# Optimization experiments

Measured on AMD Instinct MI355X. Metric: run time of the kernel, lower is better.

Reference implementation:

```python
import jax, jax.numpy as jnp
import numpy as np

H = 16  # num_heads

def setup_inputs() -> dict:
    key = jax.random.key(0)
    ks = jax.random.split(key, 9)
    B, S, E = 2, 2048, 1024
    d = E // H  # 64, shared KV head dim
    sc = lambda n: 1.0 / np.sqrt(n)
    return {
        "x": jax.random.normal(ks[0], (B, S, E), jnp.float32),
        "wq": jax.random.normal(ks[1], (E, E), jnp.float32) * sc(E),
        "bq": jax.random.normal(ks[2], (E,), jnp.float32) * 0.02,
        "wk": jax.random.normal(ks[3], (E, d), jnp.float32) * sc(E),
        "bk": jax.random.normal(ks[4], (d,), jnp.float32) * 0.02,
        "wv": jax.random.normal(ks[5], (E, d), jnp.float32) * sc(E),
        "bv": jax.random.normal(ks[6], (d,), jnp.float32) * 0.02,
        "wo": jax.random.normal(ks[7], (E, E), jnp.float32) * sc(E),
        "bo": jax.random.normal(ks[8], (E,), jnp.float32) * 0.02,
    }

def reference(x, wq, bq, wk, bk, wv, bv, wo, bo):
    B, S, E = x.shape
    d = E // H
    Q = (x @ wq + bq).reshape(B, S, H, d).transpose(0, 2, 1, 3)  # [B,H,S,d]
    K = x @ wk + bk  # [B,S,d] shared across heads (MQA)
    V = x @ wv + bv  # [B,S,d]
    scores = jnp.einsum('bhqd,bkd->bhqk', Q, K) / np.sqrt(d)  # [B,H,S,S]
    weights = jax.nn.softmax(scores, axis=-1)
    attn = jnp.einsum('bhqk,bkd->bhqd', weights, V)  # [B,H,S,d]
    # FAITHFUL to source: reshape [B,H,S,d] -> [B,S,E] WITHOUT permuting back
    attn = attn.reshape(B, S, E)
    return attn @ wo + bo
```

## Files before the change

### kernel.cpp

```cpp
#include <hip/hip_runtime.h>
#include <hip/hip_bf16.h>

#define BB 2
#define SS 2048
#define EE 1024
#define HH 16
#define DD 64

using bfrag = __attribute__((ext_vector_type(8))) short;
using ffrag = __attribute__((ext_vector_type(4))) float;

static __device__ __forceinline__ ushort f2bf(float f) {
  __hip_bfloat16 h = __float2bfloat16(f);
  return *reinterpret_cast<ushort*>(&h);
}

static __device__ __forceinline__ uint pack_bf2(float lo, float hi) {
  uint a = __float_as_uint(lo) + 0x8000u;
  uint b = __float_as_uint(hi) + 0x8000u;
  return __builtin_amdgcn_perm(b, a, 0x07060302u);
}

static __device__ __forceinline__ void gl_lds16(const ushort* g, ushort* l) {
  __builtin_amdgcn_global_load_lds(
      (const __attribute__((address_space(1))) void*)g,
      (__attribute__((address_space(3))) void*)l, 16, 0, 0);
}

__global__ __launch_bounds__(256) void cast_bf16_4(
    const float* __restrict__ src, ushort* __restrict__ dst, int n4) {
  int i = blockIdx.x * 256 + threadIdx.x;
  if (i < n4) {
    float4 v = ((const float4*)src)[i];
    ushort4 u = { f2bf(v.x), f2bf(v.y), f2bf(v.z), f2bf(v.w) };
    ((ushort4*)dst)[i] = u;
  }
}

__global__ __launch_bounds__(256) void transpose_cast(
    const float* __restrict__ src, ushort* __restrict__ dst, int K, int N) {
  __shared__ float t[32][33];
  const int k0 = blockIdx.y * 32, n0 = blockIdx.x * 32;
  const int tx = threadIdx.x & 31, ty = threadIdx.x >> 5;
  #pragma unroll
  for (int i = 0; i < 32; i += 8)
    t[ty + i][tx] = src[(size_t)(k0 + ty + i) * N + n0 + tx];
  __syncthreads();
  #pragma unroll
  for (int i = 0; i < 32; i += 8)
    dst[(size_t)(n0 + ty + i) * K + k0 + tx] = f2bf(t[tx][ty + i]);
}

template <bool QKV>
__global__ __launch_bounds__(256) void gemm_mfma3(
    const ushort* __restrict__ A, const ushort* __restrict__ Bt,
    const float* __restrict__ bias0, const float* __restrict__ bias1,
    const float* __restrict__ bias2, void* __restrict__ O1,
    ushort* __restrict__ O2, int M, int N, int K, float qscale) {
  __shared__ __align__(16) ushort As[2][128 * 64];
  __shared__ __align__(16) ushort Bs[2][64 * 64];
  const int tid = threadIdx.x;
  const int lane = tid & 63;
  const int quad = lane >> 4;
  const int c = lane & 15;
  const int wv = tid >> 6;
  const int wm = (wv & 1) * 64;
  const int wn = (wv >> 1) * 32;
  const size_t m0 = (size_t)blockIdx.y * 128;
  const size_t n0 = (size_t)blockIdx.x * 64;

  const int srow = lane >> 3;
  const int sck = (lane & 7) ^ srow;

  ffrag zero = {0.f, 0.f, 0.f, 0.f};
  ffrag acc[4][2];
  #pragma unroll
  for (int mt = 0; mt < 4; ++mt)
    #pragma unroll
    for (int nt = 0; nt < 2; ++nt) acc[mt][nt] = zero;

  const int NK = K >> 6;
  #pragma unroll
  for (int i = 0; i < 4; ++i) {
    int ia = wv * 4 + i;
    gl_lds16(&A[(m0 + ia * 8 + srow) * (size_t)K + sck * 8], &As[0][ia * 512]);
  }
  #pragma unroll
  for (int i = 0; i < 2; ++i) {
    int ib = wv * 2 + i;
    gl_lds16(&Bt[(n0 + ib * 8 + srow) * (size_t)K + sck * 8], &Bs[0][ib * 512]);
  }
  __syncthreads();

  for (int ki = 0; ki < NK; ++ki) {
    const int buf = ki & 1;
    if (ki + 1 < NK) {
      int k0 = (ki + 1) << 6;
      #pragma unroll
      for (int i = 0; i < 4; ++i) {
        int ia = wv * 4 + i;
        gl_lds16(&A[(m0 + ia * 8 + srow) * (size_t)K + k0 + sck * 8],
                 &As[buf ^ 1][ia * 512]);
      }
      #pragma unroll
      for (int i = 0; i < 2; ++i) {
        int ib = wv * 2 + i;
        gl_lds16(&Bt[(n0 + ib * 8 + srow) * (size_t)K + k0 + sck * 8],
                 &Bs[buf ^ 1][ib * 512]);
      }
    }
    #pragma unroll
    for (int ks = 0; ks < 2; ++ks) {
      bfrag af[4], bf[2];
      #pragma unroll
      for (int mt = 0; mt < 4; ++mt) {
        int ra = wm + mt * 16 + c;
        af[mt] = *(const bfrag*)&As[buf][(ra * 8 + ((ks * 4 + quad) ^ (ra & 7))) * 8];
      }
      #pragma unroll
      for (int nt = 0; nt < 2; ++nt) {
        int rb = wn + nt * 16 + c;
        bf[nt] = *(const bfrag*)&Bs[buf][(rb * 8 + ((ks * 4 + quad) ^ (rb & 7))) * 8];
      }
      #pragma unroll
      for (int mt = 0; mt < 4; ++mt)
        #pragma unroll
        for (int nt = 0; nt < 2; ++nt)
          acc[mt][nt] = __builtin_amdgcn_mfma_f32_16x16x32_bf16(
              af[mt], bf[nt], acc[mt][nt], 0, 0, 0);
    }
    __syncthreads();
  }

  #pragma unroll
  for (int nt = 0; nt < 2; ++nt) {
    const int colb = (int)n0 + wn + nt * 16;
    if (QKV) {
      float bb, sc;
      ushort* dst;
      int ldw;
      if (colb < 1024) {
        bb = bias0[colb + c]; sc = qscale;
        dst = (ushort*)O1 + colb; ldw = 1024;
      } else if (colb < 1088) {
        bb = bias1[colb - 1024 + c]; sc = 1.f;
        dst = O2 + (colb - 1024); ldw = 128;
      } else {
        bb = bias2[colb - 1088 + c]; sc = 1.f;
        dst = O2 + (colb - 1024); ldw = 128;
      }
      #pragma unroll
      for (int mt = 0; mt < 4; ++mt)
        #pragma unroll
        for (int r = 0; r < 4; ++r) {
          size_t row = m0 + wm + mt * 16 + quad * 4 + r;
          dst[row * ldw + c] = f2bf((acc[mt][nt][r] + bb) * sc);
        }
    } else {
      float bb = bias0[colb + c];
      float* dst = (float*)O1;
      #pragma unroll
      for (int mt = 0; mt < 4; ++mt)
        #pragma unroll
        for (int r = 0; r < 4; ++r) {
          size_t row = m0 + wm + mt * 16 + quad * 4 + r;
          dst[row * (size_t)N + colb + c] = acc[mt][nt][r] + bb;
        }
    }
  }
}

__global__ __launch_bounds__(256) void vt_pack(
    const ushort* __restrict__ KV, ushort* __restrict__ VT) {
  __shared__ ushort t[64][65];
  const int blk = blockIdx.x;
  const int b = blk >> 5;
  const int s0 = (blk & 31) << 6;
  const int tid = threadIdx.x;
  for (int e = tid; e < 4096; e += 256) {
    int si = e >> 6, di = e & 63;
    t[si][di] = KV[((size_t)(b * SS) + s0 + si) * 128 + 64 + di];
  }
  __syncthreads();
  for (int e = tid; e < 4096; e += 256) {
    int di = e >> 6, si = e & 63;
    VT[((size_t)b * 64 + di) * SS + s0 + si] = t[si][di];
  }
}

__global__ __launch_bounds__(256, 1) void mqa_attn7(
    const ushort* __restrict__ Q, const ushort* __restrict__ KV,
    const ushort* __restrict__ VT, ushort* __restrict__ A2) {
  __shared__ __align__(16) ushort Kt[2][4096];
  __shared__ __align__(16) ushort Vt[2][4096];
  __shared__ __align__(16) ushort P[4][64 * 72];
  const int tid = threadIdx.x;
  const int lane = tid & 63;
  const int quad = lane >> 4;
  const int c = lane & 15;
  const int wv = tid >> 6;
  const int bid = blockIdx.x;
  const int b = bid >> 7;
  const int r = bid & 127;
  const int h = r >> 3;
  const int s0 = (r & 7) << 8;

  const int srow = lane >> 3;
  const int sck = (lane & 7) ^ srow;

  ffrag zero = {0.f, 0.f, 0.f, 0.f};
  bfrag ones;
  #pragma unroll
  for (int i = 0; i < 8; ++i) ones[i] = (short)16256;

  bfrag aq[4][2];
  #pragma unroll
  for (int mt = 0; mt < 4; ++mt) {
    const ushort* qp =
        Q + ((size_t)(b * SS) + s0 + wv * 64 + mt * 16 + c) * EE + h * 64 + quad * 8;
    aq[mt][0] = *(const bfrag*)qp;
    aq[mt][1] = *(const bfrag*)(qp + 32);
  }

  ffrag o[4][4];
  #pragma unroll
  for (int mt = 0; mt < 4; ++mt)
    #pragma unroll
    for (int nt = 0; nt < 4; ++nt) o[mt][nt] = zero;
  ffrag ls[4];
  #pragma unroll
  for (int mt = 0; mt < 4; ++mt) ls[mt] = zero;
  ushort* Pw = &P[wv][0];

  const ushort* KVg = KV + (size_t)b * SS * 128;
  const ushort* VTg = VT + (size_t)b * 64 * SS;
  const int i0 = wv * 2, i1 = wv * 2 + 1;
  const int r0 = i0 * 8 + srow, r1 = i1 * 8 + srow;

  gl_lds16(KVg + (size_t)r0 * 128 + sck * 8, &Kt[0][i0 * 512]);
  gl_lds16(KVg + (size_t)r1 * 128 + sck * 8, &Kt[0][i1 * 512]);
  gl_lds16(VTg + (size_t)r0 * SS + sck * 8, &Vt[0][i0 * 512]);
  gl_lds16(VTg + (size_t)r1 * SS + sck * 8, &Vt[0][i1 * 512]);
  __syncthreads();

  for (int it = 0; it < 32; ++it) {
    const int buf = it & 1;
    if (it + 1 < 32) {
      int kb = (it + 1) << 6;
      gl_lds16(KVg + (size_t)(kb + r0) * 128 + sck * 8, &Kt[buf ^ 1][i0 * 512]);
      gl_lds16(KVg + (size_t)(kb + r1) * 128 + sck * 8, &Kt[buf ^ 1][i1 * 512]);
      gl_lds16(VTg + (size_t)r0 * SS + kb + sck * 8, &Vt[buf ^ 1][i0 * 512]);
      gl_lds16(VTg + (size_t)r1 * SS + kb + sck * 8, &Vt[buf ^ 1][i1 * 512]);
    }

    #pragma unroll
    for (int kt = 0; kt < 4; ++kt) {
      int key = kt * 16 + c;
      int k7 = key & 7;
      bfrag kf0 = *(const bfrag*)&Kt[buf][(key * 8 + (quad ^ k7)) * 8];
      bfrag kf1 = *(const bfrag*)&Kt[buf][(key * 8 + ((quad + 4) ^ k7)) * 8];
      #pragma unroll
      for (int mt = 0; mt < 4; ++mt) {
        ffrag st = __builtin_amdgcn_mfma_f32_16x16x32_bf16(kf0, aq[mt][0], zero, 0, 0, 0);
        st = __builtin_amdgcn_mfma_f32_16x16x32_bf16(kf1, aq[mt][1], st, 0, 0, 0);
        float e0 = __builtin_amdgcn_exp2f(st[0]);
        float e1 = __builtin_amdgcn_exp2f(st[1]);
        float e2 = __builtin_amdgcn_exp2f(st[2]);
        float e3 = __builtin_amdgcn_exp2f(st[3]);
        uint2 pk;
        pk.x = pack_bf2(e0, e1);
        pk.y = pack_bf2(e2, e3);
        *(uint2*)&Pw[(mt * 16 + c) * 72 + kt * 16 + quad * 4] = pk;
      }
    }
    #pragma unroll
    for (int ks = 0; ks < 2; ++ks) {
      bfrag ap[4];
      #pragma unroll
      for (int mt = 0; mt < 4; ++mt)
        ap[mt] = *(const bfrag*)&Pw[(mt * 16 + c) * 72 + ks * 32 + quad * 8];
      #pragma unroll
      for (int nt = 0; nt < 4; ++nt) {
        int d = nt * 16 + c;
        bfrag vf = *(const bfrag*)&Vt[buf][(d * 8 + ((ks * 4 + quad) ^ (d & 7))) * 8];
        #pragma unroll
        for (int mt = 0; mt < 4; ++mt)
          o[mt][nt] = __builtin_amdgcn_mfma_f32_16x16x32_bf16(ap[mt], vf, o[mt][nt], 0, 0, 0);
      }
      #pragma unroll
      for (int mt = 0; mt < 4; ++mt)
        ls[mt] = __builtin_amdgcn_mfma_f32_16x16x32_bf16(ap[mt], ones, ls[mt], 0, 0, 0);
    }
    __syncthreads();
  }

  #pragma unroll
  for (int mt = 0; mt < 4; ++mt) {
    float invo[4];
    #pragma unroll
    for (int rr = 0; rr < 4; ++rr) invo[rr] = 1.f / ls[mt][rr];
    const int sp = h * 128 + (s0 >> 4) + wv * 4 + mt;
    ushort* orow = A2 + ((size_t)b * SS + sp) * EE;
    #pragma unroll
    for (int nt = 0; nt < 4; ++nt)
      #pragma unroll
      for (int rr = 0; rr < 4; ++rr)
        orow[(quad * 4 + rr) * 64 + nt * 16 + c] = f2bf(o[mt][nt][rr] * invo[rr]);
  }
}

extern "C" void kernel_launch(void* const* d_in, const int* in_sizes, int n_in,
                              void* d_out, int out_size, void* d_ws, size_t ws_size,
                              hipStream_t stream) {
  const float* x  = (const float*)d_in[0];
  const float* wq = (const float*)d_in[1];
  const float* bq = (const float*)d_in[2];
  const float* wk = (const float*)d_in[3];
  const float* bk = (const float*)d_in[4];
  const float* wv = (const float*)d_in[5];
  const float* bv = (const float*)d_in[6];
  const float* wo = (const float*)d_in[7];
  const float* bo = (const float*)d_in[8];
  float* out = (float*)d_out;

  char* w = (char*)d_ws;
  ushort* xb     = (ushort*)w;  w += (size_t)4096 * 1024 * 2;
  ushort* wqkvT  = (ushort*)w;  w += (size_t)1152 * 1024 * 2;
  ushort* woT    = (ushort*)w;  w += (size_t)1024 * 1024 * 2;
  ushort* Qb     = (ushort*)w;  w += (size_t)4096 * 1024 * 2;
  ushort* KVb    = (ushort*)w;  w += (size_t)4096 * 128 * 2;
  ushort* VTb    = (ushort*)w;  w += (size_t)BB * 64 * SS * 2;
  ushort* A2     = (ushort*)w;  w += (size_t)4096 * 1024 * 2;

  cast_bf16_4<<<4096, 256, 0, stream>>>(x, xb, 4096 * 1024 / 4);
  transpose_cast<<<dim3(32, 32), 256, 0, stream>>>(wq, wqkvT, 1024, 1024);
  transpose_cast<<<dim3(2, 32), 256, 0, stream>>>(wk, wqkvT + (size_t)1024 * 1024, 1024, 64);
  transpose_cast<<<dim3(2, 32), 256, 0, stream>>>(wv, wqkvT + (size_t)1088 * 1024, 1024, 64);
  transpose_cast<<<dim3(32, 32), 256, 0, stream>>>(wo, woT, 1024, 1024);

  const float qscale = 0.18033688011112042f;
  gemm_mfma3<true><<<dim3(18, 32), 256, 0, stream>>>(
      xb, wqkvT, bq, bk, bv, Qb, KVb, 4096, 1152, 1024, qscale);
  vt_pack<<<64, 256, 0, stream>>>(KVb, VTb);

  mqa_attn7<<<256, 256, 0, stream>>>(Qb, KVb, VTb, A2);

  gemm_mfma3<false><<<dim3(16, 32), 256, 0, stream>>>(
      A2, woT, bo, nullptr, nullptr, out, nullptr, 4096, 1024, 1024, 1.0f);
}
```

Measured before the change: 198.9 us.

## Fuse prep kernels, write V transposed from GEMM, keep P in registers in attention

The five cast/transpose launches become a single prep kernel, and the QKV GEMM epilogue writes V directly in transposed layout with K stored separately, so the vt_pack kernel goes away. The attention kernel halves rows per block (512 blocks, 32 query rows per wave) and no longer stages P through LDS. It feeds the exp'd scores straight from the S accumulator layout into 16x16x16 MFMAs, which saves LDS traffic and barriers. The cost is more MFMA instructions (the smaller K variant), more blocks re-reading K/V, and dropping the launch_bounds occupancy hint of 1.

```diff
diff --git a/kernel.cpp b/kernel.cpp
--- a/kernel.cpp
+++ b/kernel.cpp
@@ -7,8 +7,13 @@
 #define HH 16
 #define DD 64
 
-using bfrag = __attribute__((ext_vector_type(8))) short;
-using ffrag = __attribute__((ext_vector_type(4))) float;
+using bfrag  = __attribute__((ext_vector_type(8))) short;
+using bfrag4 = __attribute__((ext_vector_type(4))) short;
+using ffrag  = __attribute__((ext_vector_type(4))) float;
+using uint2v = __attribute__((ext_vector_type(2))) uint;
+
+#define MFMA32(A, B, C) __builtin_amdgcn_mfma_f32_16x16x32_bf16(A, B, C, 0, 0, 0)
+#define MFMA16(A, B, C) __builtin_amdgcn_mfma_f32_16x16x16bf16_1k(A, B, C, 0, 0, 0)
 
 static __device__ __forceinline__ ushort f2bf(float f) {
   __hip_bfloat16 h = __float2bfloat16(f);
@@ -27,20 +32,29 @@
       (__attribute__((address_space(3))) void*)l, 16, 0, 0);
 }
 
-__global__ __launch_bounds__(256) void cast_bf16_4(
-    const float* __restrict__ src, ushort* __restrict__ dst, int n4) {
-  int i = blockIdx.x * 256 + threadIdx.x;
-  if (i < n4) {
-    float4 v = ((const float4*)src)[i];
+__global__ __launch_bounds__(256) void prep(
+    const float* __restrict__ x, const float* __restrict__ wq,
+    const float* __restrict__ wk, const float* __restrict__ wv,
+    const float* __restrict__ wo, ushort* __restrict__ xb,
+    ushort* __restrict__ wqkvT, ushort* __restrict__ woT) {
+  __shared__ float t[32][33];
+  int id = blockIdx.x;
+  if (id < 4096) {
+    int i = id * 256 + threadIdx.x;
+    float4 v = ((const float4*)x)[i];
     ushort4 u = { f2bf(v.x), f2bf(v.y), f2bf(v.z), f2bf(v.w) };
-    ((ushort4*)dst)[i] = u;
-  }
-}
-
-__global__ __launch_bounds__(256) void transpose_cast(
-    const float* __restrict__ src, ushort* __restrict__ dst, int K, int N) {
-  __shared__ float t[32][33];
-  const int k0 = blockIdx.y * 32, n0 = blockIdx.x * 32;
+    ((ushort4*)xb)[i] = u;
+    return;
+  }
+  id -= 4096;
+  const float* src;
+  ushort* dst;
+  int N, bx, by;
+  if (id < 1024)      { src = wq; dst = wqkvT;                      N = 1024; bx = id & 31;          by = id >> 5; }
+  else if (id < 2048) { src = wo; dst = woT;                        N = 1024; bx = (id - 1024) & 31; by = (id - 1024) >> 5; }
+  else if (id < 2112) { src = wk; dst = wqkvT + (size_t)1024 * 1024; N = 64;  bx = (id - 2048) & 1;  by = (id - 2048) >> 1; }
+  else                { src = wv; dst = wqkvT + (size_t)1088 * 1024; N = 64;  bx = (id - 2112) & 1;  by = (id - 2112) >> 1; }
+  const int k0 = by * 32, n0 = bx * 32;
   const int tx = threadIdx.x & 31, ty = threadIdx.x >> 5;
   #pragma unroll
   for (int i = 0; i < 32; i += 8)
@@ -48,7 +62,7 @@
   __syncthreads();
   #pragma unroll
   for (int i = 0; i < 32; i += 8)
-    dst[(size_t)(n0 + ty + i) * K + k0 + tx] = f2bf(t[tx][ty + i]);
+    dst[(size_t)(n0 + ty + i) * 1024 + k0 + tx] = f2bf(t[tx][ty + i]);
 }
 
 template <bool QKV>
@@ -56,7 +70,8 @@
     const ushort* __restrict__ A, const ushort* __restrict__ Bt,
     const float* __restrict__ bias0, const float* __restrict__ bias1,
     const float* __restrict__ bias2, void* __restrict__ O1,
-    ushort* __restrict__ O2, int M, int N, int K, float qscale) {
+    ushort* __restrict__ Kb, ushort* __restrict__ VTb,
+    int M, int N, int K, float qscale) {
   __shared__ __align__(16) ushort As[2][128 * 64];
   __shared__ __align__(16) ushort Bs[2][64 * 64];
   const int tid = threadIdx.x;
@@ -126,8 +141,7 @@
       for (int mt = 0; mt < 4; ++mt)
         #pragma unroll
         for (int nt = 0; nt < 2; ++nt)
-          acc[mt][nt] = __builtin_amdgcn_mfma_f32_16x16x32_bf16(
-              af[mt], bf[nt], acc[mt][nt], 0, 0, 0);
+          acc[mt][nt] = MFMA32(af[mt], bf[nt], acc[mt][nt]);
     }
     __syncthreads();
   }
@@ -136,26 +150,40 @@
   for (int nt = 0; nt < 2; ++nt) {
     const int colb = (int)n0 + wn + nt * 16;
     if (QKV) {
-      float bb, sc;
-      ushort* dst;
-      int ldw;
       if (colb < 1024) {
-        bb = bias0[colb + c]; sc = qscale;
-        dst = (ushort*)O1 + colb; ldw = 1024;
+        float bb = bias0[colb + c];
+        ushort* dst = (ushort*)O1 + colb;
+        #pragma unroll
+        for (int mt = 0; mt < 4; ++mt)
+          #pragma unroll
+          for (int r = 0; r < 4; ++r) {
+            size_t row = m0 + wm + mt * 16 + quad * 4 + r;
+            dst[row * 1024 + c] = f2bf((acc[mt][nt][r] + bb) * qscale);
+          }
       } else if (colb < 1088) {
-        bb = bias1[colb - 1024 + c]; sc = 1.f;
-        dst = O2 + (colb - 1024); ldw = 128;
+        float bb = bias1[colb - 1024 + c];
+        ushort* dst = Kb + (colb - 1024);
+        #pragma unroll
+        for (int mt = 0; mt < 4; ++mt)
+          #pragma unroll
+          for (int r = 0; r < 4; ++r) {
+            size_t row = m0 + wm + mt * 16 + quad * 4 + r;
+            dst[row * 64 + c] = f2bf(acc[mt][nt][r] + bb);
+          }
       } else {
-        bb = bias2[colb - 1088 + c]; sc = 1.f;
-        dst = O2 + (colb - 1024); ldw = 128;
-      }
-      #pragma unroll
-      for (int mt = 0; mt < 4; ++mt)
-        #pragma unroll
-        for (int r = 0; r < 4; ++r) {
-          size_t row = m0 + wm + mt * 16 + quad * 4 + r;
-          dst[row * ldw + c] = f2bf((acc[mt][nt][r] + bb) * sc);
+        int d = colb - 1088 + c;
+        float bb = bias2[colb - 1088 + c];
+        int bidx = (int)(m0 >> 11);
+        ushort* dstv = VTb + ((size_t)(bidx * 64 + d)) * SS;
+        #pragma unroll
+        for (int mt = 0; mt < 4; ++mt) {
+          int sb = (int)(m0 & 2047) + wm + mt * 16 + quad * 4;
+          uint2v u;
+          u.x = pack_bf2(acc[mt][nt][0] + bb, acc[mt][nt][1] + bb);
+          u.y = pack_bf2(acc[mt][nt][2] + bb, acc[mt][nt][3] + bb);
+          *(uint2v*)&dstv[sb] = u;
         }
+      }
     } else {
       float bb = bias0[colb + c];
       float* dst = (float*)O1;
@@ -170,142 +198,114 @@
   }
 }
 
-__global__ __launch_bounds__(256) void vt_pack(
-    const ushort* __restrict__ KV, ushort* __restrict__ VT) {
-  __shared__ ushort t[64][65];
-  const int blk = blockIdx.x;
-  const int b = blk >> 5;
-  const int s0 = (blk & 31) << 6;
-  const int tid = threadIdx.x;
-  for (int e = tid; e < 4096; e += 256) {
-    int si = e >> 6, di = e & 63;
-    t[si][di] = KV[((size_t)(b * SS) + s0 + si) * 128 + 64 + di];
-  }
-  __syncthreads();
-  for (int e = tid; e < 4096; e += 256) {
-    int di = e >> 6, si = e & 63;
-    VT[((size_t)b * 64 + di) * SS + s0 + si] = t[si][di];
-  }
-}
-
-__global__ __launch_bounds__(256, 1) void mqa_attn7(
-    const ushort* __restrict__ Q, const ushort* __restrict__ KV,
+__global__ __launch_bounds__(256) void mqa_attn8(
+    const ushort* __restrict__ Q, const ushort* __restrict__ Kg,
     const ushort* __restrict__ VT, ushort* __restrict__ A2) {
   __shared__ __align__(16) ushort Kt[2][4096];
   __shared__ __align__(16) ushort Vt[2][4096];
-  __shared__ __align__(16) ushort P[4][64 * 72];
   const int tid = threadIdx.x;
   const int lane = tid & 63;
   const int quad = lane >> 4;
   const int c = lane & 15;
   const int wv = tid >> 6;
   const int bid = blockIdx.x;
-  const int b = bid >> 7;
-  const int r = bid & 127;
-  const int h = r >> 3;
-  const int s0 = (r & 7) << 8;
+  const int b = bid >> 8;
+  const int r = bid & 255;
+  const int h = r >> 4;
+  const int s0 = (r & 15) << 7;
 
   const int srow = lane >> 3;
   const int sck = (lane & 7) ^ srow;
 
   ffrag zero = {0.f, 0.f, 0.f, 0.f};
-  bfrag ones;
-  #pragma unroll
-  for (int i = 0; i < 8; ++i) ones[i] = (short)16256;
-
-  bfrag aq[4][2];
-  #pragma unroll
-  for (int mt = 0; mt < 4; ++mt) {
+  bfrag4 ones4;
+  #pragma unroll
+  for (int i = 0; i < 4; ++i) ones4[i] = (short)16256;
+
+  bfrag aq[2][2];
+  #pragma unroll
+  for (int mt = 0; mt < 2; ++mt) {
     const ushort* qp =
-        Q + ((size_t)(b * SS) + s0 + wv * 64 + mt * 16 + c) * EE + h * 64 + quad * 8;
+        Q + ((size_t)(b * SS) + s0 + wv * 32 + mt * 16 + c) * EE + h * 64 + quad * 8;
     aq[mt][0] = *(const bfrag*)qp;
     aq[mt][1] = *(const bfrag*)(qp + 32);
   }
 
-  ffrag o[4][4];
-  #pragma unroll
-  for (int mt = 0; mt < 4; ++mt)
+  ffrag o[2][4];
+  #pragma unroll
+  for (int mt = 0; mt < 2; ++mt)
     #pragma unroll
     for (int nt = 0; nt < 4; ++nt) o[mt][nt] = zero;
-  ffrag ls[4];
-  #pragma unroll
-  for (int mt = 0; mt < 4; ++mt) ls[mt] = zero;
-  ushort* Pw = &P[wv][0];
-
-  const ushort* KVg = KV + (size_t)b * SS * 128;
-  const ushort* VTg = VT + (size_t)b * 64 * SS;
+  ffrag ls[2] = {zero, zero};
+
+  const ushort* Kbase = Kg + (size_t)b * SS * 64;
+  const ushort* Vbase = VT + (size_t)b * 64 * SS;
   const int i0 = wv * 2, i1 = wv * 2 + 1;
   const int r0 = i0 * 8 + srow, r1 = i1 * 8 + srow;
 
-  gl_lds16(KVg + (size_t)r0 * 128 + sck * 8, &Kt[0][i0 * 512]);
-  gl_lds16(KVg + (size_t)r1 * 128 + sck * 8, &Kt[0][i1 * 512]);
-  gl_lds16(VTg + (size_t)r0 * SS + sck * 8, &Vt[0][i0 * 512]);
-  gl_lds16(VTg + (size_t)r1 * SS + sck * 8, &Vt[0][i1 * 512]);
+  gl_lds16(Kbase + (size_t)r0 * 64 + sck * 8, &Kt[0][i0 * 512]);
+  gl_lds16(Kbase + (size_t)r1 * 64 + sck * 8, &Kt[0][i1 * 512]);
+  gl_lds16(Vbase + (size_t)r0 * SS + sck * 8, &Vt[0][i0 * 512]);
+  gl_lds16(Vbase + (size_t)r1 * SS + sck * 8, &Vt[0][i1 * 512]);
   __syncthreads();
 
   for (int it = 0; it < 32; ++it) {
     const int buf = it & 1;
     if (it + 1 < 32) {
       int kb = (it + 1) << 6;
-      gl_lds16(KVg + (size_t)(kb + r0) * 128 + sck * 8, &Kt[buf ^ 1][i0 * 512]);
-      gl_lds16(KVg + (size_t)(kb + r1) * 128 + sck * 8, &Kt[buf ^ 1][i1 * 512]);
-      gl_lds16(VTg + (size_t)r0 * SS + kb + sck * 8, &Vt[buf ^ 1][i0 * 512]);
-      gl_lds16(VTg + (size_t)r1 * SS + kb + sck * 8, &Vt[buf ^ 1][i1 * 512]);
+      gl_lds16(Kbase + (size_t)(kb + r0) * 64 + sck * 8, &Kt[buf ^ 1][i0 * 512]);
+      gl_lds16(Kbase + (size_t)(kb + r1) * 64 + sck * 8, &Kt[buf ^ 1][i1 * 512]);
+      gl_lds16(Vbase + (size_t)r0 * SS + kb + sck * 8, &Vt[buf ^ 1][i0 * 512]);
+      gl_lds16(Vbase + (size_t)r1 * SS + kb + sck * 8, &Vt[buf ^ 1][i1 * 512]);
     }
 
     #pragma unroll
     for (int kt = 0; kt < 4; ++kt) {
-      int key = kt * 16 + c;
-      int k7 = key & 7;
+      const int key = kt * 16 + c;
+      const int k7 = key & 7;
       bfrag kf0 = *(const bfrag*)&Kt[buf][(key * 8 + (quad ^ k7)) * 8];
       bfrag kf1 = *(const bfrag*)&Kt[buf][(key * 8 + ((quad + 4) ^ k7)) * 8];
-      #pragma unroll
-      for (int mt = 0; mt < 4; ++mt) {
-        ffrag st = __builtin_amdgcn_mfma_f32_16x16x32_bf16(kf0, aq[mt][0], zero, 0, 0, 0);
-        st = __builtin_amdgcn_mfma_f32_16x16x32_bf16(kf1, aq[mt][1], st, 0, 0, 0);
-        float e0 = __builtin_amdgcn_exp2f(st[0]);
-        float e1 = __builtin_amdgcn_exp2f(st[1]);
-        float e2 = __builtin_amdgcn_exp2f(st[2]);
-        float e3 = __builtin_amdgcn_exp2f(st[3]);
-        uint2 pk;
-        pk.x = pack_bf2(e0, e1);
-        pk.y = pack_bf2(e2, e3);
-        *(uint2*)&Pw[(mt * 16 + c) * 72 + kt * 16 + quad * 4] = pk;
-      }
-    }
-    #pragma unroll
-    for (int ks = 0; ks < 2; ++ks) {
-      bfrag ap[4];
-      #pragma unroll
-      for (int mt = 0; mt < 4; ++mt)
-        ap[mt] = *(const bfrag*)&Pw[(mt * 16 + c) * 72 + ks * 32 + quad * 8];
+      bfrag4 pb[2];
+      #pragma unroll
+      for (int mt = 0; mt < 2; ++mt) {
+        ffrag st = MFMA32(kf0, aq[mt][0], zero);
+        st = MFMA32(kf1, aq[mt][1], st);
+        uint2v uu;
+        uu.x = pack_bf2(__builtin_amdgcn_exp2f(st[0]),
+                        __builtin_amdgcn_exp2f(st[1]));
+        uu.y = pack_bf2(__builtin_amdgcn_exp2f(st[2]),
+                        __builtin_amdgcn_exp2f(st[3]));
+        pb[mt] = __builtin_bit_cast(bfrag4, uu);
+      }
+      const int ck = kt * 2 + (quad >> 1);
+      const int wc = (quad & 1) * 4;
       #pragma unroll
       for (int nt = 0; nt < 4; ++nt) {
         int d = nt * 16 + c;
-        bfrag vf = *(const bfrag*)&Vt[buf][(d * 8 + ((ks * 4 + quad) ^ (d & 7))) * 8];
-        #pragma unroll
-        for (int mt = 0; mt < 4; ++mt)
-          o[mt][nt] = __builtin_amdgcn_mfma_f32_16x16x32_bf16(ap[mt], vf, o[mt][nt], 0, 0, 0);
-      }
-      #pragma unroll
-      for (int mt = 0; mt < 4; ++mt)
-        ls[mt] = __builtin_amdgcn_mfma_f32_16x16x32_bf16(ap[mt], ones, ls[mt], 0, 0, 0);
+        bfrag4 vf = *(const bfrag4*)&Vt[buf][(d * 8 + (ck ^ (d & 7))) * 8 + wc];
+        #pragma unroll
+        for (int mt = 0; mt < 2; ++mt)
+          o[mt][nt] = MFMA16(vf, pb[mt], o[mt][nt]);
+      }
+      #pragma unroll
+      for (int mt = 0; mt < 2; ++mt)
+        ls[mt] = MFMA16(ones4, pb[mt], ls[mt]);
     }
     __syncthreads();
   }
 
   #pragma unroll
-  for (int mt = 0; mt < 4; ++mt) {
-    float invo[4];
-    #pragma unroll
-    for (int rr = 0; rr < 4; ++rr) invo[rr] = 1.f / ls[mt][rr];
-    const int sp = h * 128 + (s0 >> 4) + wv * 4 + mt;
+  for (int mt = 0; mt < 2; ++mt) {
+    const float inv = 1.f / ls[mt][0];
+    const int sp = h * 128 + (s0 >> 4) + wv * 2 + mt;
     ushort* orow = A2 + ((size_t)b * SS + sp) * EE;
     #pragma unroll
-    for (int nt = 0; nt < 4; ++nt)
-      #pragma unroll
-      for (int rr = 0; rr < 4; ++rr)
-        orow[(quad * 4 + rr) * 64 + nt * 16 + c] = f2bf(o[mt][nt][rr] * invo[rr]);
+    for (int nt = 0; nt < 4; ++nt) {
+      uint2v u;
+      u.x = pack_bf2(o[mt][nt][0] * inv, o[mt][nt][1] * inv);
+      u.y = pack_bf2(o[mt][nt][2] * inv, o[mt][nt][3] * inv);
+      *(uint2v*)&orow[c * 64 + nt * 16 + quad * 4] = u;
+    }
   }
 }
 
@@ -328,23 +328,18 @@
   ushort* wqkvT  = (ushort*)w;  w += (size_t)1152 * 1024 * 2;
   ushort* woT    = (ushort*)w;  w += (size_t)1024 * 1024 * 2;
   ushort* Qb     = (ushort*)w;  w += (size_t)4096 * 1024 * 2;
-  ushort* KVb    = (ushort*)w;  w += (size_t)4096 * 128 * 2;
+  ushort* Kb     = (ushort*)w;  w += (size_t)4096 * 64 * 2;
   ushort* VTb    = (ushort*)w;  w += (size_t)BB * 64 * SS * 2;
   ushort* A2     = (ushort*)w;  w += (size_t)4096 * 1024 * 2;
 
-  cast_bf16_4<<<4096, 256, 0, stream>>>(x, xb, 4096 * 1024 / 4);
-  transpose_cast<<<dim3(32, 32), 256, 0, stream>>>(wq, wqkvT, 1024, 1024);
-  transpose_cast<<<dim3(2, 32), 256, 0, stream>>>(wk, wqkvT + (size_t)1024 * 1024, 1024, 64);
-  transpose_cast<<<dim3(2, 32), 256, 0, stream>>>(wv, wqkvT + (size_t)1088 * 1024, 1024, 64);
-  transpose_cast<<<dim3(32, 32), 256, 0, stream>>>(wo, woT, 1024, 1024);
+  prep<<<6272, 256, 0, stream>>>(x, wq, wk, wv, wo, xb, wqkvT, woT);
 
   const float qscale = 0.18033688011112042f;
   gemm_mfma3<true><<<dim3(18, 32), 256, 0, stream>>>(
-      xb, wqkvT, bq, bk, bv, Qb, KVb, 4096, 1152, 1024, qscale);
-  vt_pack<<<64, 256, 0, stream>>>(KVb, VTb);
-
-  mqa_attn7<<<256, 256, 0, stream>>>(Qb, KVb, VTb, A2);
+      xb, wqkvT, bq, bk, bv, Qb, Kb, VTb, 4096, 1152, 1024, qscale);
+
+  mqa_attn8<<<512, 256, 0, stream>>>(Qb, Kb, VTb, A2);
 
   gemm_mfma3<false><<<dim3(16, 32), 256, 0, stream>>>(
-      A2, woT, bo, nullptr, nullptr, out, nullptr, 4096, 1024, 1024, 1.0f);
-}
+      A2, woT, bo, nullptr, nullptr, out, nullptr, nullptr, 4096, 1024, 1024, 1.0f);
+}
```

After: 183.2 us. 1.09x faster.
